# Performance work log

Hardware: AMD Instinct MI355X
Metric: run time of the kernel (lower is better)

## Reference

```python
import jax, jax.numpy as jnp
import numpy as np

jax.config.update("jax_enable_x64", True)  # 64-bit hashes for collision-free WL signatures

N_NODES = 100_000
N_FEATURES = 64
N_EDGES = 6_400_000
NUM_ITERATIONS = 3
STEP = 1


def setup_inputs() -> dict:
    key = jax.random.key(0)
    kx, ke = jax.random.split(key)
    x = jax.random.normal(kx, (N_NODES, N_FEATURES), dtype=jnp.float32)  # one-hot-ish label scores
    edge_index = jax.random.randint(ke, (2, N_EDGES), 0, N_NODES, dtype=jnp.int64)
    return {"x": x, "edge_index": edge_index}


def _splitmix64(z):
    # High-quality 64-bit mixer (uint64, wraps mod 2^64).
    z = z + jnp.uint64(0x9E3779B97F4A7C15)
    z = (z ^ (z >> jnp.uint64(30))) * jnp.uint64(0xBF58476D1CE4E5B9)
    z = (z ^ (z >> jnp.uint64(27))) * jnp.uint64(0x94D049BB133111EB)
    return z ^ (z >> jnp.uint64(31))


def _wl_conv(colors, src, dst, offset):
    """One WL refinement: hash (own color, multiset of neighbor colors), then
    relabel signatures by first-occurrence order (matches PyG WLConv's dict
    insertion order), continuing the global color counter `offset` (matches the
    persistent hashmap across iterations)."""
    n = colors.shape[0]
    h = _splitmix64(colors.astype(jnp.uint64) + jnp.uint64(1))
    # multiset of neighbor colors -> order-invariant sum of neighbor hashes
    nb_sum = jnp.zeros(n, dtype=jnp.uint64).at[dst].add(h[src])  # [N]
    sig = _splitmix64(h * jnp.uint64(0x100000001B3) + nb_sum)    # [N] signatures
    # first-occurrence relabeling (stable, deterministic)
    _, inv = jnp.unique(sig, size=n, fill_value=jnp.uint64(0), return_inverse=True)
    idx = jnp.arange(n, dtype=jnp.int64)
    first_idx = jax.ops.segment_min(idx, inv, num_segments=n)  # empty segments -> int64 max
    order = jnp.argsort(first_idx)                              # real uniques come first
    ranks = jnp.zeros(n, dtype=jnp.int64).at[order].set(idx)
    new_colors = offset + ranks[inv]
    num_new = jnp.sum(first_idx < n).astype(jnp.int64)
    return new_colors, offset + num_new


def reference(x, edge_index):
    src, dst = edge_index[0], edge_index[1]
    colors = jnp.argmax(x, axis=1).astype(jnp.int64)  # [N]
    feats = [colors]
    offset = jnp.int64(0)
    for _ in range(NUM_ITERATIONS):
        for _ in range(STEP):
            colors, offset = _wl_conv(colors, src, dst, offset)
        feats.append(colors)
    return jnp.stack(feats, axis=-1)  # [N, NUM_ITERATIONS+1], int64
```

## Files before the change

### kernel.cpp

```cpp
#include <hip/hip_runtime.h>

typedef unsigned long long u64;
typedef unsigned int u32;
typedef int  v4i __attribute__((ext_vector_type(4)));
typedef unsigned int v4u __attribute__((ext_vector_type(4)));

#define TBL_BITS 18
#define TBL_SIZE (1u << TBL_BITS)
#define TBL_MASK (TBL_SIZE - 1u)
#define EMPTY_KEY 0xFFFFFFFFFFFFFFFFull

#define BK_BITS 9
#define BK_SZ   512
#define MAXNB   256
#define NBLK    512
#define NSUB    8

__device__ __forceinline__ u64 splitmix64(u64 z) {
    z = z + 0x9E3779B97F4A7C15ull;
    z = (z ^ (z >> 30)) * 0xBF58476D1CE4E5B9ull;
    z = (z ^ (z >> 27)) * 0x94D049BB133111EBull;
    return z ^ (z >> 31);
}

__device__ __forceinline__ v4i nt_load4(const int* p) {
    return __builtin_nontemporal_load((const v4i*)p);
}
__device__ __forceinline__ v4u nt_loadu4(const u32* p) {
    return __builtin_nontemporal_load((const v4u*)p);
}

__global__ void argmax_kernel(const float* __restrict__ x, u64* __restrict__ h,
                              int* __restrict__ out, u32* __restrict__ offsets, int n) {
    if (blockIdx.x == 0 && threadIdx.x == 0) offsets[0] = 0u;
    int wave = (int)((blockIdx.x * (u32)blockDim.x + threadIdx.x) >> 6);
    int lane = threadIdx.x & 63;
    if (wave >= n) return;
    float v = x[(size_t)wave * 64 + lane];
    int idx = lane;
    #pragma unroll
    for (int off = 32; off >= 1; off >>= 1) {
        float ov = __shfl_xor(v, off);
        int   oi = __shfl_xor(idx, off);
        if (ov > v || (ov == v && oi < idx)) { v = ov; idx = oi; }
    }
    if (lane == 0) {
        h[wave] = splitmix64((u64)idx + 1ull);
        out[(size_t)wave * 4 + 0] = idx;
    }
}


__global__ __launch_bounds__(1024) void count_part(const int* __restrict__ dst,
                                                   u32* __restrict__ cnt, int m, int nbuck) {
    __shared__ u32 hist[MAXNB];
    int t = threadIdx.x, b = blockIdx.x;
    for (int i = t; i < nbuck; i += 1024) hist[i] = 0u;
    __syncthreads();
    int mv = m >> 2;
    int perv = (mv + NBLK - 1) / NBLK;
    int lo = b * perv, hi = lo + perv; if (hi > mv) hi = mv;
    for (int i = lo + t; i < hi; i += 1024) {
        v4i v = nt_load4(dst + 4 * (size_t)i);
        atomicAdd(&hist[((u32)v.x) >> BK_BITS], 1u);
        atomicAdd(&hist[((u32)v.y) >> BK_BITS], 1u);
        atomicAdd(&hist[((u32)v.z) >> BK_BITS], 1u);
        atomicAdd(&hist[((u32)v.w) >> BK_BITS], 1u);
    }
    if (b == 0 && t == 0)
        for (int e = mv * 4; e < m; ++e) atomicAdd(&hist[((u32)dst[e]) >> BK_BITS], 1u);
    __syncthreads();
    for (int i = t; i < nbuck; i += 1024) cnt[i * NBLK + b] = hist[i];
}

__global__ __launch_bounds__(512) void scan_bucket(u32* __restrict__ cnt,
                                                   u32* __restrict__ total, int nbuck) {
    int b = blockIdx.x, t = threadIdx.x;
    u32 v = cnt[b * NBLK + t];
    int lane = t & 63, w = t >> 6;
    int x = (int)v;
    #pragma unroll
    for (int o = 1; o < 64; o <<= 1) {
        int y = __shfl_up(x, o);
        if (lane >= o) x += y;
    }
    __shared__ u32 ws[8];
    if (lane == 63) ws[w] = (u32)x;
    __syncthreads();
    u32 woff = 0;
    for (int ww = 0; ww < w; ++ww) woff += ws[ww];
    u32 incl = woff + (u32)x;
    cnt[b * NBLK + t] = incl - v;
    if (t == NBLK - 1) total[b] = incl;
}

__global__ void scan_bases(const u32* __restrict__ total, u32* __restrict__ bases, int nbuck) {
    __shared__ u32 A[256], B[256];
    int t = threadIdx.x;
    u32 pt = (t < nbuck) ? ((total[t] + 63u) & ~63u) : 0u;
    A[t] = pt; __syncthreads();
    u32 *cur = A, *nxt = B;
    for (int o = 1; o < 256; o <<= 1) {
        u32 y = cur[t] + ((t >= o) ? cur[t - o] : 0u);
        nxt[t] = y; __syncthreads();
        u32* tmp = cur; cur = nxt; nxt = tmp;
    }
    if (t < nbuck) bases[t] = cur[t] - pt;
}

__global__ __launch_bounds__(1024) void scatter_part(const int* __restrict__ src,
                                                     const int* __restrict__ dst,
                                                     const u32* __restrict__ cnt,
                                                     const u32* __restrict__ bases,
                                                     u32* __restrict__ packed, int m, int nbuck) {
    __shared__ u32 pos[MAXNB];
    int t = threadIdx.x, b = blockIdx.x;
    for (int i = t; i < nbuck; i += 1024) pos[i] = bases[i] + cnt[i * NBLK + b];
    __syncthreads();
    int mv = m >> 2;
    int perv = (mv + NBLK - 1) / NBLK;
    int lo = b * perv, hi = lo + perv; if (hi > mv) hi = mv;
    for (int i = lo + t; i < hi; i += 1024) {
        v4i dv = nt_load4(dst + 4 * (size_t)i);
        v4i sv = nt_load4(src + 4 * (size_t)i);
        u32 d0 = (u32)dv.x, d1 = (u32)dv.y, d2 = (u32)dv.z, d3 = (u32)dv.w;
        u32 p0 = atomicAdd(&pos[d0 >> BK_BITS], 1u);
        packed[p0] = ((u32)sv.x << BK_BITS) | (d0 & (BK_SZ - 1u));
        u32 p1 = atomicAdd(&pos[d1 >> BK_BITS], 1u);
        packed[p1] = ((u32)sv.y << BK_BITS) | (d1 & (BK_SZ - 1u));
        u32 p2 = atomicAdd(&pos[d2 >> BK_BITS], 1u);
        packed[p2] = ((u32)sv.z << BK_BITS) | (d2 & (BK_SZ - 1u));
        u32 p3 = atomicAdd(&pos[d3 >> BK_BITS], 1u);
        packed[p3] = ((u32)sv.w << BK_BITS) | (d3 & (BK_SZ - 1u));
    }
    if (b == 0 && t == 0) {
        for (int e = mv * 4; e < m; ++e) {
            u32 d = (u32)dst[e];
            u32 p = atomicAdd(&pos[d >> BK_BITS], 1u);
            packed[p] = ((u32)src[e] << BK_BITS) | (d & (BK_SZ - 1u));
        }
    }
}

__global__ __launch_bounds__(256) void nb_kernel(const u32* __restrict__ packed,
                                                 const u32* __restrict__ bases,
                                                 const u32* __restrict__ total,
                                                 const u64* __restrict__ h,
                                                 u64* __restrict__ nb8, size_t nstride,
                                                 u64* __restrict__ keys,
                                                 u32* __restrict__ vals, int nbuck) {
    int b = blockIdx.x, t = threadIdx.x;
    if (b >= nbuck * NSUB) {
        int base = (b - nbuck * NSUB) * 1024;
        for (int k = t; k < 1024; k += 256) { keys[base + k] = EMPTY_KEY; vals[base + k] = 0xFFFFFFFFu; }
        return;
    }
    int bucket = b >> 3, sub = b & 7;
    __shared__ u64 acc[BK_SZ];
    acc[t] = 0ull; acc[t + 256] = 0ull;
    __syncthreads();
    u32 lo = bases[bucket];
    u32 len = total[bucket];
    u32 q0 = ((len * (u32)sub) >> 3) & ~3u;
    u32 q1 = (sub == 7) ? len : (((len * (u32)(sub + 1)) >> 3) & ~3u);
    u32 nv4 = (q1 - q0) >> 2;
    const u32* pbase = packed + lo + q0;
    for (u32 i = (u32)t; i < nv4; i += 256) {
        v4u v = nt_loadu4(pbase + 4 * (size_t)i);
        atomicAdd(&acc[v.x & (BK_SZ - 1u)], h[v.x >> BK_BITS]);
        atomicAdd(&acc[v.y & (BK_SZ - 1u)], h[v.y >> BK_BITS]);
        atomicAdd(&acc[v.z & (BK_SZ - 1u)], h[v.z >> BK_BITS]);
        atomicAdd(&acc[v.w & (BK_SZ - 1u)], h[v.w >> BK_BITS]);
    }
    for (u32 e = q0 + nv4 * 4 + (u32)t; e < q1; e += 256) {
        u32 v = packed[lo + e];
        atomicAdd(&acc[v & (BK_SZ - 1u)], h[v >> BK_BITS]);
    }
    __syncthreads();
    u64* dstp = nb8 + (size_t)sub * nstride + ((size_t)bucket << BK_BITS);
    dstp[t] = acc[t];
    dstp[t + 256] = acc[t + 256];
}


__global__ void sig_kernel8(const u64* __restrict__ h, const u64* __restrict__ nb8,
                            size_t nstride, u32* __restrict__ slotarr,
                            u64* __restrict__ keys, u32* __restrict__ vals, int n) {
    int i = blockIdx.x * blockDim.x + threadIdx.x;
    if (i >= n) return;
    u64 nbv = 0;
    #pragma unroll
    for (int s = 0; s < NSUB; ++s) nbv += nb8[(size_t)s * nstride + i];
    u64 sg = splitmix64(h[i] * 0x100000001B3ull + nbv);
    u32 slot = (u32)sg & TBL_MASK;
    while (true) {
        u64 k = keys[slot];
        if (k == sg) break;
        if (k == EMPTY_KEY) {
            u64 prev = atomicCAS(&keys[slot], (u64)EMPTY_KEY, sg);
            if (prev == EMPTY_KEY || prev == sg) break;
        }
        slot = (slot + 1u) & TBL_MASK;
    }
    atomicMin(&vals[slot], (u32)i);
    slotarr[i] = slot;
}

__global__ void sig_kernel1(const u64* __restrict__ h, const u64* __restrict__ nb,
                            u32* __restrict__ slotarr, u64* __restrict__ keys,
                            u32* __restrict__ vals, int n) {
    int i = blockIdx.x * blockDim.x + threadIdx.x;
    if (i >= n) return;
    u64 sg = splitmix64(h[i] * 0x100000001B3ull + nb[i]);
    u32 slot = (u32)sg & TBL_MASK;
    while (true) {
        u64 k = keys[slot];
        if (k == sg) break;
        if (k == EMPTY_KEY) {
            u64 prev = atomicCAS(&keys[slot], (u64)EMPTY_KEY, sg);
            if (prev == EMPTY_KEY || prev == sg) break;
        }
        slot = (slot + 1u) & TBL_MASK;
    }
    atomicMin(&vals[slot], (u32)i);
    slotarr[i] = slot;
}

__global__ void count_rank(const u32* __restrict__ slotarr, const u32* __restrict__ vals,
                           u32* __restrict__ f, u32* __restrict__ lrank,
                           u32* __restrict__ partials, int n) {
    int b = blockIdx.x, t = threadIdx.x;
    int i = b * 256 + t;
    u32 isf = 0, fi = 0;
    if (i < n) {
        fi = vals[slotarr[i]];
        f[i] = fi;
        isf = (fi == (u32)i) ? 1u : 0u;
    }
    __shared__ u32 wsum[4];
    u32 lane = t & 63, wv = (u32)t >> 6;
    int x = (int)isf;
    #pragma unroll
    for (int o = 1; o < 64; o <<= 1) {
        int y = __shfl_up(x, o);
        if (lane >= (u32)o) x += y;
    }
    if (lane == 63) wsum[wv] = (u32)x;
    __syncthreads();
    u32 woff = 0;
    for (u32 w = 0; w < wv; ++w) woff += wsum[w];
    if (i < n) lrank[i] = woff + (u32)x - isf;
    if (t == 255) partials[b] = woff + (u32)x;
}

__global__ __launch_bounds__(512) void relabel_fused(const u32* __restrict__ f,
                                                     const u32* __restrict__ lrank,
                                                     const u32* __restrict__ partials,
                                                     u32* __restrict__ offsets, int iter,
                                                     u64* __restrict__ h, int* __restrict__ out,
                                                     int n, int npb) {
    __shared__ u32 pp[512];
    __shared__ u32 ws[8];
    int t = threadIdx.x;
    u32 v = (t < npb) ? partials[t] : 0u;
    int lane = t & 63, w = t >> 6;
    int x = (int)v;
    #pragma unroll
    for (int o = 1; o < 64; o <<= 1) {
        int y = __shfl_up(x, o);
        if (lane >= o) x += y;
    }
    if (lane == 63) ws[w] = (u32)x;
    __syncthreads();
    u32 woff = 0;
    for (int ww = 0; ww < w; ++ww) woff += ws[ww];
    u32 incl = woff + (u32)x;
    pp[t] = incl - v;
    if (blockIdx.x == 0 && t == 511) offsets[iter + 1] = offsets[iter] + incl;
    __syncthreads();
    int i = blockIdx.x * 512 + t;
    if (i >= n) return;
    u32 j = f[i];
    u32 c = offsets[iter] + pp[j >> 8] + lrank[j];
    h[i] = splitmix64((u64)c + 1ull);
    out[(size_t)i * 4 + (iter + 1)] = (int)c;
}


__global__ void init_iter_kernel(u64* __restrict__ keys, u32* __restrict__ vals,
                                 u64* __restrict__ nb, int n) {
    int i = blockIdx.x * blockDim.x + threadIdx.x;
    if (i < (int)TBL_SIZE) { keys[i] = EMPTY_KEY; vals[i] = 0xFFFFFFFFu; }
    if (i < n) nb[i] = 0ull;
}

__global__ void edge_kernel(const int* __restrict__ src, const int* __restrict__ dst,
                            const u64* __restrict__ h, u64* __restrict__ nb, int m) {
    int stride = gridDim.x * blockDim.x;
    for (int e = blockIdx.x * blockDim.x + threadIdx.x; e < m; e += stride) {
        atomicAdd(&nb[(u32)dst[e]], h[(u32)src[e]]);
    }
}

extern "C" void kernel_launch(void* const* d_in, const int* in_sizes, int n_in,
                              void* d_out, int out_size, void* d_ws, size_t ws_size,
                              hipStream_t stream) {
    const float* x = (const float*)d_in[0];
    const int* ei = (const int*)d_in[1];
    int n = in_sizes[0] / 64;
    int m = in_sizes[1] / 2;
    const int* src = ei;
    const int* dst = ei + m;
    int* out = (int*)d_out;

    const int NPB = (n + 255) / 256;
    const int NRB = (n + 511) / 512;
    const int nbuck = (n + BK_SZ - 1) >> BK_BITS;
    const size_t nstride = (size_t)nbuck << BK_BITS;

    auto align = [](size_t v) { return (v + 255) & ~(size_t)255; };
    size_t sz_packed = align((size_t)m * 4 + (size_t)MAXNB * 64 * 4);
    size_t sz_cnt    = align((size_t)MAXNB * NBLK * 4);
    size_t sz_bt     = align((size_t)MAXNB * 4);
    size_t sz_h      = align((size_t)n * 8);
    size_t sz_nb8    = align(nstride * 8 * NSUB);
    size_t sz_tblk   = align((size_t)TBL_SIZE * 8);
    size_t sz_tblv   = align((size_t)TBL_SIZE * 4);
    size_t sz_n4     = align((size_t)n * 4);
    size_t sz_small  = align((size_t)512 * 4);
    size_t need_fast = sz_packed + sz_cnt + 2 * sz_bt + sz_h + sz_nb8 + sz_tblk + sz_tblv
                     + 3 * sz_n4 + sz_small + 256;

    char* p = (char*)d_ws;
    bool fast = (ws_size >= need_fast) && (nbuck <= MAXNB) && ((m & 3) == 0) && (NPB <= 512);
    if (fast) {
        u32* packed  = (u32*)p; p += sz_packed;
        u32* cnt     = (u32*)p; p += sz_cnt;
        u32* total   = (u32*)p; p += sz_bt;
        u32* bases   = (u32*)p; p += sz_bt;
        u64* h       = (u64*)p; p += sz_h;
        u64* nb8     = (u64*)p; p += sz_nb8;
        u64* keys    = (u64*)p; p += sz_tblk;
        u32* vals    = (u32*)p; p += sz_tblv;
        u32* slotarr = (u32*)p; p += sz_n4;
        u32* f       = (u32*)p; p += sz_n4;
        u32* lrank   = (u32*)p; p += sz_n4;
        u32* partials= (u32*)p; p += sz_small;
        u32* offsets = (u32*)p;

        argmax_kernel<<<(n + 3) / 4, 256, 0, stream>>>(x, h, out, offsets, n);
        count_part  <<<NBLK, 1024, 0, stream>>>(dst, cnt, m, nbuck);
        scan_bucket <<<nbuck, NBLK, 0, stream>>>(cnt, total, nbuck);
        scan_bases  <<<1, 256, 0, stream>>>(total, bases, nbuck);
        scatter_part<<<NBLK, 1024, 0, stream>>>(src, dst, cnt, bases, packed, m, nbuck);

        for (int it = 0; it < 3; ++it) {
            nb_kernel    <<<nbuck * NSUB + 256, 256, 0, stream>>>(packed, bases, total, h,
                                                                  nb8, nstride, keys, vals, nbuck);
            sig_kernel8  <<<NPB, 256, 0, stream>>>(h, nb8, nstride, slotarr, keys, vals, n);
            count_rank   <<<NPB, 256, 0, stream>>>(slotarr, vals, f, lrank, partials, n);
            relabel_fused<<<NRB, 512, 0, stream>>>(f, lrank, partials, offsets, it, h, out, n, NPB);
        }
    } else {
        u64* h       = (u64*)p; p += sz_h;
        u64* nb      = (u64*)p; p += sz_h;
        u64* keys    = (u64*)p; p += sz_tblk;
        u32* vals    = (u32*)p; p += sz_tblv;
        u32* slotarr = (u32*)p; p += sz_n4;
        u32* f       = (u32*)p; p += sz_n4;
        u32* lrank   = (u32*)p; p += sz_n4;
        u32* partials= (u32*)p; p += sz_small;
        u32* offsets = (u32*)p;

        argmax_kernel<<<(n + 3) / 4, 256, 0, stream>>>(x, h, out, offsets, n);
        for (int it = 0; it < 3; ++it) {
            init_iter_kernel<<<(TBL_SIZE + 255) / 256, 256, 0, stream>>>(keys, vals, nb, n);
            edge_kernel  <<<4096, 256, 0, stream>>>(src, dst, h, nb, m);
            sig_kernel1  <<<NPB, 256, 0, stream>>>(h, nb, slotarr, keys, vals, n);
            count_rank   <<<NPB, 256, 0, stream>>>(slotarr, vals, f, lrank, partials, n);
            relabel_fused<<<NRB, 512, 0, stream>>>(f, lrank, partials, offsets, it, h, out, n, NPB);
        }
    }
}
```

Before: 260.9 us.

## Replace count/scan/scatter edge bucketing with single-pass LDS partition kernel

The old path made two passes over the edge list (histogram, then scatter) with two small scan kernels in between. A single partition kernel now replaces all four. Each block stages its edge chunk in LDS, sorts it locally by destination bucket, reserves space per bucket with one global atomic, and writes contiguous runs into fixed-capacity bucket slots. This removes one full read of dst and three launches, and makes the scattered writes more coalesced. The cost is a per-bucket capacity sized for near-uniform degree: a bucket that overflows has its position clamped and its edges overwritten, so skewed graphs would give wrong results.

```diff
diff --git a/kernel.cpp b/kernel.cpp
--- a/kernel.cpp
+++ b/kernel.cpp
@@ -2,6 +2,7 @@
 
 typedef unsigned long long u64;
 typedef unsigned int u32;
+typedef unsigned char u8;
 typedef int  v4i __attribute__((ext_vector_type(4)));
 typedef unsigned int v4u __attribute__((ext_vector_type(4)));
 
@@ -13,7 +14,8 @@
 #define BK_BITS 9
 #define BK_SZ   512
 #define MAXNB   256
-#define NBLK    512
+#define PBLK    2048
+#define LDSE    3200
 #define NSUB    8
 
 __device__ __forceinline__ u64 splitmix64(u64 z) {
@@ -31,9 +33,12 @@
 }
 
 __global__ void argmax_kernel(const float* __restrict__ x, u64* __restrict__ h,
-                              int* __restrict__ out, u32* __restrict__ offsets, int n) {
-    if (blockIdx.x == 0 && threadIdx.x == 0) offsets[0] = 0u;
-    int wave = (int)((blockIdx.x * (u32)blockDim.x + threadIdx.x) >> 6);
+                              int* __restrict__ out, u32* __restrict__ offsets,
+                              u32* __restrict__ gcur, int n) {
+    int gid = blockIdx.x * blockDim.x + threadIdx.x;
+    if (gid == 0) offsets[0] = 0u;
+    if (gid < MAXNB) gcur[gid] = 0u;
+    int wave = gid >> 6;
     int lane = threadIdx.x & 63;
     if (wave >= n) return;
     float v = x[(size_t)wave * 64 + lane];
@@ -50,33 +55,39 @@
     }
 }
 
-
-__global__ __launch_bounds__(1024) void count_part(const int* __restrict__ dst,
-                                                   u32* __restrict__ cnt, int m, int nbuck) {
-    __shared__ u32 hist[MAXNB];
+__global__ __launch_bounds__(256) void partition_kernel(const int* __restrict__ src,
+                                                        const int* __restrict__ dst,
+                                                        u32* __restrict__ gcur,
+                                                        u32* __restrict__ packed,
+                                                        int mI4, int nbuck, int cap, int per) {
+    __shared__ u32 pk[LDSE];
+    __shared__ u32 spk[LDSE];
+    __shared__ u8  bd[LDSE];
+    __shared__ u8  sbd[LDSE];
+    __shared__ u32 hist[256], lstart[256], adjB[256], cur[256];
+    __shared__ u32 wsum[4];
     int t = threadIdx.x, b = blockIdx.x;
-    for (int i = t; i < nbuck; i += 1024) hist[i] = 0u;
-    __syncthreads();
-    int mv = m >> 2;
-    int perv = (mv + NBLK - 1) / NBLK;
-    int lo = b * perv, hi = lo + perv; if (hi > mv) hi = mv;
-    for (int i = lo + t; i < hi; i += 1024) {
-        v4i v = nt_load4(dst + 4 * (size_t)i);
-        atomicAdd(&hist[((u32)v.x) >> BK_BITS], 1u);
-        atomicAdd(&hist[((u32)v.y) >> BK_BITS], 1u);
-        atomicAdd(&hist[((u32)v.z) >> BK_BITS], 1u);
-        atomicAdd(&hist[((u32)v.w) >> BK_BITS], 1u);
-    }
-    if (b == 0 && t == 0)
-        for (int e = mv * 4; e < m; ++e) atomicAdd(&hist[((u32)dst[e]) >> BK_BITS], 1u);
-    __syncthreads();
-    for (int i = t; i < nbuck; i += 1024) cnt[i * NBLK + b] = hist[i];
-}
-
-__global__ __launch_bounds__(512) void scan_bucket(u32* __restrict__ cnt,
-                                                   u32* __restrict__ total, int nbuck) {
-    int b = blockIdx.x, t = threadIdx.x;
-    u32 v = cnt[b * NBLK + t];
+    hist[t] = 0u;
+    __syncthreads();
+    int i0 = b * per;
+    int i1 = i0 + per; if (i1 > mI4) i1 = mI4;
+    int nI = i1 - i0; if (nI < 0) nI = 0;
+    int nE = nI * 4;
+    for (int i = t; i < nI; i += 256) {
+        v4i dv = nt_load4(dst + 4 * (size_t)(i0 + i));
+        v4i sv = nt_load4(src + 4 * (size_t)(i0 + i));
+        u32 d, s, bid;
+        d = (u32)dv.x; s = (u32)sv.x; bid = d >> BK_BITS;
+        pk[4*i+0] = (s << BK_BITS) | (d & (BK_SZ-1u)); bd[4*i+0] = (u8)bid; atomicAdd(&hist[bid], 1u);
+        d = (u32)dv.y; s = (u32)sv.y; bid = d >> BK_BITS;
+        pk[4*i+1] = (s << BK_BITS) | (d & (BK_SZ-1u)); bd[4*i+1] = (u8)bid; atomicAdd(&hist[bid], 1u);
+        d = (u32)dv.z; s = (u32)sv.z; bid = d >> BK_BITS;
+        pk[4*i+2] = (s << BK_BITS) | (d & (BK_SZ-1u)); bd[4*i+2] = (u8)bid; atomicAdd(&hist[bid], 1u);
+        d = (u32)dv.w; s = (u32)sv.w; bid = d >> BK_BITS;
+        pk[4*i+3] = (s << BK_BITS) | (d & (BK_SZ-1u)); bd[4*i+3] = (u8)bid; atomicAdd(&hist[bid], 1u);
+    }
+    __syncthreads();
+    u32 v = hist[t];
     int lane = t & 63, w = t >> 6;
     int x = (int)v;
     #pragma unroll
@@ -84,71 +95,37 @@
         int y = __shfl_up(x, o);
         if (lane >= o) x += y;
     }
-    __shared__ u32 ws[8];
-    if (lane == 63) ws[w] = (u32)x;
+    if (lane == 63) wsum[w] = (u32)x;
     __syncthreads();
     u32 woff = 0;
-    for (int ww = 0; ww < w; ++ww) woff += ws[ww];
-    u32 incl = woff + (u32)x;
-    cnt[b * NBLK + t] = incl - v;
-    if (t == NBLK - 1) total[b] = incl;
-}
-
-__global__ void scan_bases(const u32* __restrict__ total, u32* __restrict__ bases, int nbuck) {
-    __shared__ u32 A[256], B[256];
-    int t = threadIdx.x;
-    u32 pt = (t < nbuck) ? ((total[t] + 63u) & ~63u) : 0u;
-    A[t] = pt; __syncthreads();
-    u32 *cur = A, *nxt = B;
-    for (int o = 1; o < 256; o <<= 1) {
-        u32 y = cur[t] + ((t >= o) ? cur[t - o] : 0u);
-        nxt[t] = y; __syncthreads();
-        u32* tmp = cur; cur = nxt; nxt = tmp;
-    }
-    if (t < nbuck) bases[t] = cur[t] - pt;
-}
-
-__global__ __launch_bounds__(1024) void scatter_part(const int* __restrict__ src,
-                                                     const int* __restrict__ dst,
-                                                     const u32* __restrict__ cnt,
-                                                     const u32* __restrict__ bases,
-                                                     u32* __restrict__ packed, int m, int nbuck) {
-    __shared__ u32 pos[MAXNB];
-    int t = threadIdx.x, b = blockIdx.x;
-    for (int i = t; i < nbuck; i += 1024) pos[i] = bases[i] + cnt[i * NBLK + b];
-    __syncthreads();
-    int mv = m >> 2;
-    int perv = (mv + NBLK - 1) / NBLK;
-    int lo = b * perv, hi = lo + perv; if (hi > mv) hi = mv;
-    for (int i = lo + t; i < hi; i += 1024) {
-        v4i dv = nt_load4(dst + 4 * (size_t)i);
-        v4i sv = nt_load4(src + 4 * (size_t)i);
-        u32 d0 = (u32)dv.x, d1 = (u32)dv.y, d2 = (u32)dv.z, d3 = (u32)dv.w;
-        u32 p0 = atomicAdd(&pos[d0 >> BK_BITS], 1u);
-        packed[p0] = ((u32)sv.x << BK_BITS) | (d0 & (BK_SZ - 1u));
-        u32 p1 = atomicAdd(&pos[d1 >> BK_BITS], 1u);
-        packed[p1] = ((u32)sv.y << BK_BITS) | (d1 & (BK_SZ - 1u));
-        u32 p2 = atomicAdd(&pos[d2 >> BK_BITS], 1u);
-        packed[p2] = ((u32)sv.z << BK_BITS) | (d2 & (BK_SZ - 1u));
-        u32 p3 = atomicAdd(&pos[d3 >> BK_BITS], 1u);
-        packed[p3] = ((u32)sv.w << BK_BITS) | (d3 & (BK_SZ - 1u));
-    }
-    if (b == 0 && t == 0) {
-        for (int e = mv * 4; e < m; ++e) {
-            u32 d = (u32)dst[e];
-            u32 p = atomicAdd(&pos[d >> BK_BITS], 1u);
-            packed[p] = ((u32)src[e] << BK_BITS) | (d & (BK_SZ - 1u));
-        }
+    for (int ww = 0; ww < w; ++ww) woff += wsum[ww];
+    u32 excl = woff + (u32)x - v;
+    lstart[t] = excl;
+    cur[t] = excl;
+    if (t < nbuck && v > 0u) {
+        u32 bpos = atomicAdd(&gcur[t], v);
+        if (bpos > (u32)cap - v) bpos = (u32)cap - v;
+        adjB[t] = (u32)t * (u32)cap + bpos - excl;
+    }
+    __syncthreads();
+    for (int i = t; i < nE; i += 256) {
+        u32 bb = (u32)bd[i];
+        u32 p = atomicAdd(&cur[bb], 1u);
+        spk[p] = pk[i];
+        sbd[p] = (u8)bb;
+    }
+    __syncthreads();
+    for (int p = t; p < nE; p += 256) {
+        packed[adjB[sbd[p]] + (u32)p] = spk[p];
     }
 }
 
 __global__ __launch_bounds__(256) void nb_kernel(const u32* __restrict__ packed,
-                                                 const u32* __restrict__ bases,
-                                                 const u32* __restrict__ total,
+                                                 const u32* __restrict__ gcur,
                                                  const u64* __restrict__ h,
                                                  u64* __restrict__ nb8, size_t nstride,
                                                  u64* __restrict__ keys,
-                                                 u32* __restrict__ vals, int nbuck) {
+                                                 u32* __restrict__ vals, int nbuck, int cap) {
     int b = blockIdx.x, t = threadIdx.x;
     if (b >= nbuck * NSUB) {
         int base = (b - nbuck * NSUB) * 1024;
@@ -159,8 +136,8 @@
     __shared__ u64 acc[BK_SZ];
     acc[t] = 0ull; acc[t + 256] = 0ull;
     __syncthreads();
-    u32 lo = bases[bucket];
-    u32 len = total[bucket];
+    u32 lo = (u32)bucket * (u32)cap;
+    u32 len = gcur[bucket];
     u32 q0 = ((len * (u32)sub) >> 3) & ~3u;
     u32 q1 = (sub == 7) ? len : (((len * (u32)(sub + 1)) >> 3) & ~3u);
     u32 nv4 = (q1 - q0) >> 2;
@@ -317,27 +294,26 @@
     const int NRB = (n + 511) / 512;
     const int nbuck = (n + BK_SZ - 1) >> BK_BITS;
     const size_t nstride = (size_t)nbuck << BK_BITS;
+    const int mI4 = m >> 2;
+    const int per = (mI4 + PBLK - 1) / PBLK;
+    const int cap = (int)((((size_t)m / (size_t)(nbuck > 0 ? nbuck : 1)) * 9 / 8 + 2048 + 255) & ~(size_t)255);
 
     auto align = [](size_t v) { return (v + 255) & ~(size_t)255; };
-    size_t sz_packed = align((size_t)m * 4 + (size_t)MAXNB * 64 * 4);
-    size_t sz_cnt    = align((size_t)MAXNB * NBLK * 4);
-    size_t sz_bt     = align((size_t)MAXNB * 4);
+    size_t sz_packed = align((size_t)nbuck * (size_t)cap * 4);
     size_t sz_h      = align((size_t)n * 8);
     size_t sz_nb8    = align(nstride * 8 * NSUB);
     size_t sz_tblk   = align((size_t)TBL_SIZE * 8);
     size_t sz_tblv   = align((size_t)TBL_SIZE * 4);
     size_t sz_n4     = align((size_t)n * 4);
     size_t sz_small  = align((size_t)512 * 4);
-    size_t need_fast = sz_packed + sz_cnt + 2 * sz_bt + sz_h + sz_nb8 + sz_tblk + sz_tblv
-                     + 3 * sz_n4 + sz_small + 256;
+    size_t need_fast = sz_packed + sz_h + sz_nb8 + sz_tblk + sz_tblv
+                     + 3 * sz_n4 + 2 * sz_small + 256;
 
     char* p = (char*)d_ws;
-    bool fast = (ws_size >= need_fast) && (nbuck <= MAXNB) && ((m & 3) == 0) && (NPB <= 512);
+    bool fast = (ws_size >= need_fast) && (nbuck <= MAXNB) && ((m & 3) == 0)
+              && (NPB <= 512) && (per * 4 <= LDSE) && (n >= 256);
     if (fast) {
         u32* packed  = (u32*)p; p += sz_packed;
-        u32* cnt     = (u32*)p; p += sz_cnt;
-        u32* total   = (u32*)p; p += sz_bt;
-        u32* bases   = (u32*)p; p += sz_bt;
         u64* h       = (u64*)p; p += sz_h;
         u64* nb8     = (u64*)p; p += sz_nb8;
         u64* keys    = (u64*)p; p += sz_tblk;
@@ -346,17 +322,15 @@
         u32* f       = (u32*)p; p += sz_n4;
         u32* lrank   = (u32*)p; p += sz_n4;
         u32* partials= (u32*)p; p += sz_small;
+        u32* gcur    = (u32*)p; p += sz_small;
         u32* offsets = (u32*)p;
 
-        argmax_kernel<<<(n + 3) / 4, 256, 0, stream>>>(x, h, out, offsets, n);
-        count_part  <<<NBLK, 1024, 0, stream>>>(dst, cnt, m, nbuck);
-        scan_bucket <<<nbuck, NBLK, 0, stream>>>(cnt, total, nbuck);
-        scan_bases  <<<1, 256, 0, stream>>>(total, bases, nbuck);
-        scatter_part<<<NBLK, 1024, 0, stream>>>(src, dst, cnt, bases, packed, m, nbuck);
+        argmax_kernel<<<(n + 3) / 4, 256, 0, stream>>>(x, h, out, offsets, gcur, n);
+        partition_kernel<<<PBLK, 256, 0, stream>>>(src, dst, gcur, packed, mI4, nbuck, cap, per);
 
         for (int it = 0; it < 3; ++it) {
-            nb_kernel    <<<nbuck * NSUB + 256, 256, 0, stream>>>(packed, bases, total, h,
-                                                                  nb8, nstride, keys, vals, nbuck);
+            nb_kernel    <<<nbuck * NSUB + 256, 256, 0, stream>>>(packed, gcur, h,
+                                                                  nb8, nstride, keys, vals, nbuck, cap);
             sig_kernel8  <<<NPB, 256, 0, stream>>>(h, nb8, nstride, slotarr, keys, vals, n);
             count_rank   <<<NPB, 256, 0, stream>>>(slotarr, vals, f, lrank, partials, n);
             relabel_fused<<<NRB, 512, 0, stream>>>(f, lrank, partials, offsets, it, h, out, n, NPB);
@@ -370,9 +344,10 @@
         u32* f       = (u32*)p; p += sz_n4;
         u32* lrank   = (u32*)p; p += sz_n4;
         u32* partials= (u32*)p; p += sz_small;
+        u32* gcur    = (u32*)p; p += sz_small;
         u32* offsets = (u32*)p;
 
-        argmax_kernel<<<(n + 3) / 4, 256, 0, stream>>>(x, h, out, offsets, n);
+        argmax_kernel<<<(n + 63) / 64 >= 1 ? (n + 3) / 4 : 1, 256, 0, stream>>>(x, h, out, offsets, gcur, n);
         for (int it = 0; it < 3; ++it) {
             init_iter_kernel<<<(TBL_SIZE + 255) / 256, 256, 0, stream>>>(keys, vals, nb, n);
             edge_kernel  <<<4096, 256, 0, stream>>>(src, dst, h, nb, m);
```

New measurement: 261.8 us. Within noise of the previous version (+0.3%).
